# Performance work log

Hardware: AMD Instinct MI355X
Metric: run time of the kernel (lower is better)

The kernel has to match this reference:

```python
import jax, jax.numpy as jnp
import numpy as np

L, N, E, H, D, F = 2048, 2, 1024, 16, 64, 4096  # seq, batch, embed, heads, head_dim, ffn
EPS = 1e-5


def _ln(x, w, b):
    m = jnp.mean(x, axis=-1, keepdims=True)
    v = jnp.mean(jnp.square(x - m), axis=-1, keepdims=True)
    return (x - m) * jax.lax.rsqrt(v + EPS) * w + b


def setup_inputs() -> dict:
    key = jax.random.key(0)
    ks = jax.random.split(key, 16)
    s = 0.02
    f32 = jnp.float32
    return {
        "x": jax.random.normal(ks[0], (L, N, E), f32),
        "ln1_w": jnp.ones((E,), f32),
        "ln1_b": jnp.zeros((E,), f32),
        "wq": jax.random.normal(ks[1], (H * D, E), f32) * s,
        "bq": jnp.zeros((H * D,), f32),
        "wk": jax.random.normal(ks[2], (H * D, E), f32) * s,
        "bk": jnp.zeros((H * D,), f32),
        "wv": jax.random.normal(ks[3], (H * D, E), f32) * s,
        "bv": jnp.zeros((H * D,), f32),
        "wout": jax.random.normal(ks[4], (E, H * D), f32) * s,
        "bout": jnp.zeros((E,), f32),
        "ln2_w": jnp.ones((E,), f32),
        "ln2_b": jnp.zeros((E,), f32),
        "fc1_w": jax.random.normal(ks[5], (F, E), f32) * s,
        "fc1_b": jnp.zeros((F,), f32),
        "fc2_w": jax.random.normal(ks[6], (E, F), f32) * s,
        "fc2_b": jnp.zeros((E,), f32),
    }


def reference(x, ln1_w, ln1_b, wq, bq, wk, bk, wv, bv, wout, bout,
              ln2_w, ln2_b, fc1_w, fc1_b, fc2_w, fc2_b):
    scale = D ** (-0.5)
    residual = x
    h = _ln(x, ln1_w, ln1_b)                      # (L,N,E)
    q = (h @ wq.T + bq).reshape(L, N, H, D) * scale
    k = (h @ wk.T + bk).reshape(L, N, H, D)
    v = (h @ wv.T + bv).reshape(L, N, H, D)
    attn = jnp.einsum('qnhd,knhd->nhqk', q, k)    # (N,H,L,L) full score matrix
    causal = jnp.tril(jnp.ones((L, L), bool))
    attn = jnp.where(causal[None, None], attn, jnp.float32(-10000.0))
    p = jax.nn.softmax(attn, axis=-1)
    o = jnp.einsum('nhqk,knhd->qnhd', p, v).reshape(L, N, H * D)
    o = o @ wout.T + bout
    x = o + residual
    residual = x
    h = _ln(x, ln2_w, ln2_b)
    h = jax.nn.gelu(h @ fc1_w.T + fc1_b, approximate=False)
    h = h @ fc2_w.T + fc2_b
    return h + residual
```

## Files before the change

### kernel.cpp

```cpp
#include <hip/hip_runtime.h>
#include <hip/hip_bf16.h>
#include <math.h>

using bf16 = __hip_bfloat16;
typedef __bf16 bf16x8 __attribute__((ext_vector_type(8)));
typedef short  short4v __attribute__((ext_vector_type(4)));
typedef float  f32x4  __attribute__((ext_vector_type(4)));

static constexpr int Lq = 2048, Nb = 2, E = 1024, Hh = 16, Dd = 64, Ff = 4096;
static constexpr int MT = Lq * Nb;
static constexpr int QKLD = 2 * E;
static constexpr int LDL = 2 * QKLD;

__device__ __forceinline__ void async_lds16(const void* g, void* l) {
  __builtin_amdgcn_global_load_lds(
      (const __attribute__((address_space(1))) void*)g,
      (__attribute__((address_space(3))) void*)l, 16, 0, 0);
}
__device__ __forceinline__ bf16x8 ld8(const bf16* p) { return *(const bf16x8*)p; }
__device__ __forceinline__ short bfbits(float x) {
  bf16 t = __float2bfloat16(x);
  return *(short*)&t;
}

__global__ __launch_bounds__(256) void cvt_all_kernel(
    const float* __restrict__ wq, const float* __restrict__ wk,
    const float* __restrict__ wv, const float* __restrict__ wout,
    const float* __restrict__ fc1w, const float* __restrict__ fc2w,
    bf16* __restrict__ wqkvb, bf16* __restrict__ woutb,
    bf16* __restrict__ f1wb, bf16* __restrict__ f2wb) {
  const int i = blockIdx.x * 256 + threadIdx.x;
  const float* src;
  bf16* dst;
  size_t off;
  if (i < 786432) {
    const int r = i >> 18;
    off = (size_t)(i & 262143);
    src = (r == 0) ? wq : (r == 1) ? wk : wv;
    dst = wqkvb + (size_t)r * (E * E);
  } else if (i < 1048576) {
    off = (size_t)(i - 786432); src = wout; dst = woutb;
  } else if (i < 2097152) {
    off = (size_t)(i - 1048576); src = fc1w; dst = f1wb;
  } else {
    off = (size_t)(i - 2097152); src = fc2w; dst = f2wb;
  }
  float4 v = ((const float4*)src)[off];
  bf16 o4[4] = {__float2bfloat16(v.x), __float2bfloat16(v.y),
                __float2bfloat16(v.z), __float2bfloat16(v.w)};
  *(uint2*)(dst + 4 * off) = *(uint2*)o4;
}

template <int EPI>
__global__ __launch_bounds__(256) void gemm_bt(
    const bf16* __restrict__ A, const bf16* __restrict__ W,
    const float* __restrict__ b1, const float* __restrict__ b2,
    const float* __restrict__ b3, int Klen, int Kstride, int Nld,
    float qscale, int scut, bf16* __restrict__ outb,
    bf16* __restrict__ outv) {
  __shared__ __align__(16) bf16 As[128 * 32];
  __shared__ __align__(16) bf16 Bs[128 * 32];
  const int tid = threadIdx.x;
  const int w = tid >> 6, lane = tid & 63;
  const int quad = lane >> 4, l16 = lane & 15;
  const int wm = (w >> 1) * 64, wn = (w & 1) * 64;
  const int m0 = blockIdx.y * 128, n0 = blockIdx.x * 128;
  const int koff = blockIdx.z * Klen;

  f32x4 acc[4][4];
#pragma unroll
  for (int i = 0; i < 4; i++)
#pragma unroll
    for (int j = 0; j < 4; j++)
#pragma unroll
      for (int r = 0; r < 4; r++) acc[i][j][r] = 0.f;

  const int c0 = w * 64 + lane;
  const int c1 = c0 + 256;
  const size_t arow0 = (size_t)(m0 + (c0 >> 2)), arow1 = (size_t)(m0 + (c1 >> 2));
  const size_t brow0 = (size_t)(n0 + (c0 >> 2)), brow1 = (size_t)(n0 + (c1 >> 2));
  const int col0 = (c0 & 3) * 8, col1 = (c1 & 3) * 8;
  bf16* ldsA0 = &As[(w * 64) * 8];
  bf16* ldsA1 = &As[(256 + w * 64) * 8];
  bf16* ldsB0 = &Bs[(w * 64) * 8];
  bf16* ldsB1 = &Bs[(256 + w * 64) * 8];

  const int nk = Klen >> 5;
  for (int kt = 0; kt < nk; ++kt) {
    const int k0 = koff + kt * 32;
    async_lds16(A + arow0 * Kstride + k0 + col0, ldsA0);
    async_lds16(A + arow1 * Kstride + k0 + col1, ldsA1);
    async_lds16(W + brow0 * Kstride + k0 + col0, ldsB0);
    async_lds16(W + brow1 * Kstride + k0 + col1, ldsB1);
    __syncthreads();
    bf16x8 a[4], b[4];
#pragma unroll
    for (int i = 0; i < 4; i++) {
      a[i] = ld8(&As[(wm + i * 16 + l16) * 32 + quad * 8]);
      b[i] = ld8(&Bs[(wn + i * 16 + l16) * 32 + quad * 8]);
    }
#pragma unroll
    for (int i = 0; i < 4; i++)
#pragma unroll
      for (int j = 0; j < 4; j++)
        acc[i][j] = __builtin_amdgcn_mfma_f32_16x16x32_bf16(a[i], b[j], acc[i][j], 0, 0, 0);
    __syncthreads();
  }

  const size_t zoff = (EPI == 3) ? (size_t)blockIdx.z * ((size_t)MT * E) : 0;
#pragma unroll
  for (int i = 0; i < 4; i++) {
    const int mrow = m0 + wm + i * 16 + quad * 4;
#pragma unroll
    for (int j = 0; j < 4; j++) {
      const int ncol = n0 + wn + j * 16 + l16;
      float bv = 0.f;
      if constexpr (EPI != 3) {
        if (b3 != nullptr) {
          bv = (ncol < 1024) ? b1[ncol]
               : (ncol < 2048) ? b2[ncol - 1024] : b3[ncol - 2048];
        } else {
          bv = b1[ncol];
        }
      }
      const float sc = (ncol < scut) ? qscale : 1.0f;
#pragma unroll
      for (int r = 0; r < 4; r++) {
        float v = (acc[i][j][r] + bv) * sc;
        if constexpr (EPI == 2) {
          v = 0.5f * v * (1.f + erff(v * 0.70710678118f));
          outb[(size_t)(mrow + r) * Nld + ncol] = __float2bfloat16(v);
        } else if constexpr (EPI == 3) {
          outb[zoff + (size_t)(mrow + r) * Nld + ncol] = __float2bfloat16(v);
        } else {
          if (ncol < 2048) {
            outb[(size_t)(mrow + r) * 2048 + ncol] = __float2bfloat16(v);
          } else {
            const int h = (ncol - 2048) >> 6, d = ncol & 63;
            const int tok = mrow + r, n = tok & 1, l = tok >> 1;
            outv[(size_t)((n * 16 + h) * 64 + d) * Lq + l] = __float2bfloat16(v);
          }
        }
      }
    }
  }
}

__global__ __launch_bounds__(256) void reduce2_kernel(
    const bf16* __restrict__ P, const float* __restrict__ bias,
    const float* __restrict__ res, float* __restrict__ out) {
  const int i = blockIdx.x * 256 + threadIdx.x;
  const size_t e0 = (size_t)i * 4;
  const int col = (int)(e0 & (E - 1));
  uint2 u0 = *(const uint2*)(P + e0);
  uint2 u1 = *(const uint2*)(P + (size_t)MT * E + e0);
  const bf16* p0 = (const bf16*)&u0;
  const bf16* p1 = (const bf16*)&u1;
  float4 b = *(const float4*)(bias + col);
  float4 r = *(const float4*)(res + e0);
  float4 o;
  o.x = (float)p0[0] + (float)p1[0] + b.x + r.x;
  o.y = (float)p0[1] + (float)p1[1] + b.y + r.y;
  o.z = (float)p0[2] + (float)p1[2] + b.z + r.z;
  o.w = (float)p0[3] + (float)p1[3] + b.w + r.w;
  *(float4*)(out + e0) = o;
}

__global__ __launch_bounds__(256) void ln_kernel(
    const float* __restrict__ x, const float* __restrict__ wgt,
    const float* __restrict__ bia, bf16* __restrict__ out) {
  const int t = blockIdx.x, tid = threadIdx.x;
  const size_t base = (size_t)t * E;
  float v4[4], s = 0.f, ss = 0.f;
#pragma unroll
  for (int i = 0; i < 4; i++) {
    float v = x[base + i * 256 + tid];
    v4[i] = v; s += v; ss += v * v;
  }
  for (int off = 32; off > 0; off >>= 1) {
    s += __shfl_down(s, off, 64);
    ss += __shfl_down(ss, off, 64);
  }
  __shared__ float rs[4], rss[4], mv[2];
  const int w = tid >> 6;
  if ((tid & 63) == 0) { rs[w] = s; rss[w] = ss; }
  __syncthreads();
  if (tid == 0) {
    float S = rs[0] + rs[1] + rs[2] + rs[3];
    float SS = rss[0] + rss[1] + rss[2] + rss[3];
    float mean = S * (1.f / E);
    float var = SS * (1.f / E) - mean * mean;
    mv[0] = mean; mv[1] = rsqrtf(var + 1e-5f);
  }
  __syncthreads();
  const float mean = mv[0], rstd = mv[1];
#pragma unroll
  for (int i = 0; i < 4; i++) {
    const int e = i * 256 + tid;
    float r = (v4[i] - mean) * rstd * wgt[e] + bia[e];
    out[base + e] = __float2bfloat16(r);
  }
}

__global__ __launch_bounds__(256) void attn_kernel(
    const bf16* __restrict__ QK, const bf16* __restrict__ VT,
    bf16* __restrict__ O) {
  __shared__ __align__(16) bf16 KB[512 * 8];
  __shared__ __align__(16) bf16 VB[512 * 8];
  const int tid = threadIdx.x;
  const int w = tid >> 6, lane = tid & 63, quad = lane >> 4, l16 = lane & 15;
  const int pid = blockIdx.x;
  const int hh = blockIdx.y;
  const int n = hh >> 4, h = hh & 15;

  const bf16* Qp = QK + n * QKLD + h * Dd;
  const bf16* Kp = Qp + E;
  const bf16* Vp = VT + (size_t)hh * 64 * Lq;

  bf16* ldsK0 = KB + (size_t)(w * 64) * 8;
  bf16* ldsK1 = KB + (size_t)(256 + w * 64) * 8;
  bf16* ldsV0 = VB + (size_t)(w * 64) * 8;
  bf16* ldsV1 = VB + (size_t)(256 + w * 64) * 8;
  const int w8 = w * 8;

  for (int half = 0; half < 2; ++half) {
    const int qt = (half == 0) ? (31 - pid) : pid;
    const int ql = qt * 64 + w * 16 + l16;
    const bf16x8 aq0 = ld8(Qp + (size_t)ql * LDL + quad * 8);
    const bf16x8 aq1 = ld8(Qp + (size_t)ql * LDL + 32 + quad * 8);

    f32x4 o_acc[4];
#pragma unroll
    for (int d = 0; d < 4; d++)
#pragma unroll
      for (int r = 0; r < 4; r++) o_acc[d][r] = 0.f;
    float m_run = -3e30f, l_run = 0.f;

    for (int kt = 0; kt <= qt; ++kt) {
      const size_t kb = (size_t)kt * 64;

      async_lds16(Kp + (size_t)(kb + lane) * LDL + w8, ldsK0);
      async_lds16(Kp + (size_t)(kb + lane) * LDL + 32 + w8, ldsK1);
      async_lds16(Vp + (size_t)lane * Lq + kb + w8, ldsV0);
      async_lds16(Vp + (size_t)lane * Lq + kb + 32 + w8, ldsV1);
      __syncthreads();

      f32x4 s[4];
#pragma unroll
      for (int ks = 0; ks < 4; ks++) {
        const bf16x8 kc0 = ld8(&KB[(size_t)((quad)*64 + ks * 16 + l16) * 8]);
        const bf16x8 kc1 = ld8(&KB[(size_t)((4 + quad) * 64 + ks * 16 + l16) * 8]);
#pragma unroll
        for (int r = 0; r < 4; r++) s[ks][r] = 0.f;
        s[ks] = __builtin_amdgcn_mfma_f32_16x16x32_bf16(kc0, aq0, s[ks], 0, 0, 0);
        s[ks] = __builtin_amdgcn_mfma_f32_16x16x32_bf16(kc1, aq1, s[ks], 0, 0, 0);
      }

      if (kt == qt) {
#pragma unroll
        for (int ks = 0; ks < 4; ks++) {
#pragma unroll
          for (int r = 0; r < 4; r++) {
            const int kg = kt * 64 + ks * 16 + quad * 4 + r;
            if (kg > ql) s[ks][r] = -14427.0f;
          }
        }
      }

      float tmax = s[0][0];
#pragma unroll
      for (int ks = 0; ks < 4; ks++)
#pragma unroll
        for (int r = 0; r < 4; r++) tmax = fmaxf(tmax, s[ks][r]);
      tmax = fmaxf(tmax, __shfl_xor(tmax, 16, 64));
      tmax = fmaxf(tmax, __shfl_xor(tmax, 32, 64));
      const float mnew = fmaxf(m_run, tmax);
      const float alpha = exp2f(m_run - mnew);
      m_run = mnew;
      float rsum = 0.f;
      short4v pf[4];
#pragma unroll
      for (int ks = 0; ks < 4; ks++) {
#pragma unroll
        for (int r = 0; r < 4; r++) {
          const float pv = exp2f(s[ks][r] - mnew);
          rsum += pv;
          pf[ks][r] = bfbits(pv);
        }
      }
      rsum += __shfl_xor(rsum, 16, 64);
      rsum += __shfl_xor(rsum, 32, 64);
      l_run = l_run * alpha + rsum;
#pragma unroll
      for (int d = 0; d < 4; d++)
#pragma unroll
        for (int r = 0; r < 4; r++) o_acc[d][r] *= alpha;

#pragma unroll
      for (int d = 0; d < 4; d++) {
#pragma unroll
        for (int ks = 0; ks < 4; ks++) {
          const int g = ks * 2 + (quad >> 1);
          const short4v av =
              *(const short4v*)&VB[(size_t)(g * 64 + d * 16 + l16) * 8 + (quad & 1) * 4];
          o_acc[d] = __builtin_amdgcn_mfma_f32_16x16x16bf16_1k(av, pf[ks], o_acc[d], 0, 0, 0);
        }
      }
      __syncthreads();
    }

    const float inv_l = 1.f / fmaxf(l_run, 1e-30f);
    const size_t obase = (size_t)ql * (Nb * E) + (size_t)n * E + h * Dd;
#pragma unroll
    for (int d = 0; d < 4; d++)
#pragma unroll
      for (int r = 0; r < 4; r++)
        O[obase + d * 16 + quad * 4 + r] = __float2bfloat16(o_acc[d][r] * inv_l);
  }
}

extern "C" void kernel_launch(void* const* d_in, const int* in_sizes, int n_in,
                              void* d_out, int out_size, void* d_ws, size_t ws_size,
                              hipStream_t stream) {
  const float* x    = (const float*)d_in[0];
  const float* ln1w = (const float*)d_in[1];
  const float* ln1b = (const float*)d_in[2];
  const float* wq   = (const float*)d_in[3];
  const float* bq   = (const float*)d_in[4];
  const float* wk   = (const float*)d_in[5];
  const float* bk   = (const float*)d_in[6];
  const float* wv   = (const float*)d_in[7];
  const float* bv   = (const float*)d_in[8];
  const float* wout = (const float*)d_in[9];
  const float* bout = (const float*)d_in[10];
  const float* ln2w = (const float*)d_in[11];
  const float* ln2b = (const float*)d_in[12];
  const float* fc1w = (const float*)d_in[13];
  const float* fc1b = (const float*)d_in[14];
  const float* fc2w = (const float*)d_in[15];
  const float* fc2b = (const float*)d_in[16];

  char* ws = (char*)d_ws;
  bf16* wqkvb = (bf16*)(ws);
  bf16* woutb = (bf16*)(ws + ((size_t)6 << 20));
  bf16* f1wb  = (bf16*)(ws + ((size_t)8 << 20));
  bf16* f2wb  = (bf16*)(ws + ((size_t)16 << 20));
  bf16* h1    = (bf16*)(ws + ((size_t)24 << 20));
  bf16* qk    = (bf16*)(ws + ((size_t)32 << 20));
  bf16* vtg   = (bf16*)(ws + ((size_t)48 << 20));
  bf16* o     = (bf16*)(ws + ((size_t)56 << 20));
  float* x1   = (float*)(ws + ((size_t)64 << 20));
  bf16* Pout  = (bf16*)(ws + ((size_t)32 << 20));
  bf16* P01   = (bf16*)(ws);
  bf16* f1    = (bf16*)(ws + ((size_t)32 << 20));
  bf16* h2    = h1;
  float* outp = (float*)d_out;

  cvt_all_kernel<<<12288, 256, 0, stream>>>(wq, wk, wv, wout, fc1w, fc2w,
                                            wqkvb, woutb, f1wb, f2wb);

  ln_kernel<<<MT, 256, 0, stream>>>(x, ln1w, ln1b, h1);

  dim3 gQKV(3 * E / 128, MT / 128);
  dim3 gE2(E / 128, MT / 128, 2);
  dim3 gF(Ff / 128, MT / 128);

  gemm_bt<4><<<gQKV, 256, 0, stream>>>(h1, wqkvb, bq, bk, bv, E, E, 2048,
                                       0.125f * 1.44269504f, 1024, qk, vtg);

  attn_kernel<<<dim3(16, Nb * Hh), 256, 0, stream>>>(qk, vtg, o);

  gemm_bt<3><<<gE2, 256, 0, stream>>>(o, woutb, nullptr, nullptr, nullptr,
                                      E / 2, E, E, 1.f, 0, Pout, nullptr);
  reduce2_kernel<<<MT * E / 1024, 256, 0, stream>>>(Pout, bout, x, x1);

  ln_kernel<<<MT, 256, 0, stream>>>(x1, ln2w, ln2b, h2);

  gemm_bt<2><<<gF, 256, 0, stream>>>(h2, f1wb, fc1b, nullptr, nullptr, E, E, Ff,
                                     1.f, 0, f1, nullptr);

  gemm_bt<3><<<gE2, 256, 0, stream>>>(f1, f2wb, nullptr, nullptr, nullptr,
                                      Ff / 2, Ff, E, 1.f, 0, P01, nullptr);
  reduce2_kernel<<<MT * E / 1024, 256, 0, stream>>>(P01, fc2b, x1, outp);
}
```

Before: 423.2 us.

## Deepen GEMM K-tile with swizzled LDS, fuse reduce+LN2, use tanh-form GELU

```diff
diff --git a/kernel.cpp b/kernel.cpp
--- a/kernel.cpp
+++ b/kernel.cpp
@@ -21,6 +21,11 @@
 __device__ __forceinline__ short bfbits(float x) {
   bf16 t = __float2bfloat16(x);
   return *(short*)&t;
+}
+__device__ __forceinline__ float gelu_fast(float v) {
+  const float y = fminf(2.302208f * (v + 0.044715f * v * v * v), 80.f);
+  const float t = exp2f(y);
+  return v * t / (t + 1.0f);
 }
 
 __global__ __launch_bounds__(256) void cvt_all_kernel(
@@ -58,8 +63,8 @@
     const float* __restrict__ b3, int Klen, int Kstride, int Nld,
     float qscale, int scut, bf16* __restrict__ outb,
     bf16* __restrict__ outv) {
-  __shared__ __align__(16) bf16 As[128 * 32];
-  __shared__ __align__(16) bf16 Bs[128 * 32];
+  __shared__ __align__(16) bf16 As[128 * 64];
+  __shared__ __align__(16) bf16 Bs[128 * 64];
   const int tid = threadIdx.x;
   const int w = tid >> 6, lane = tid & 63;
   const int quad = lane >> 4, l16 = lane & 15;
@@ -75,35 +80,37 @@
 #pragma unroll
       for (int r = 0; r < 4; r++) acc[i][j][r] = 0.f;
 
-  const int c0 = w * 64 + lane;
-  const int c1 = c0 + 256;
-  const size_t arow0 = (size_t)(m0 + (c0 >> 2)), arow1 = (size_t)(m0 + (c1 >> 2));
-  const size_t brow0 = (size_t)(n0 + (c0 >> 2)), brow1 = (size_t)(n0 + (c1 >> 2));
-  const int col0 = (c0 & 3) * 8, col1 = (c1 & 3) * 8;
-  bf16* ldsA0 = &As[(w * 64) * 8];
-  bf16* ldsA1 = &As[(256 + w * 64) * 8];
-  bf16* ldsB0 = &Bs[(w * 64) * 8];
-  bf16* ldsB1 = &Bs[(256 + w * 64) * 8];
-
-  const int nk = Klen >> 5;
+  const int rowoff = w * 8 + (lane >> 3);
+  const int colsw = (((lane & 7) ^ (lane >> 3)) << 3);
+
+  const int nk = Klen >> 6;
   for (int kt = 0; kt < nk; ++kt) {
-    const int k0 = koff + kt * 32;
-    async_lds16(A + arow0 * Kstride + k0 + col0, ldsA0);
-    async_lds16(A + arow1 * Kstride + k0 + col1, ldsA1);
-    async_lds16(W + brow0 * Kstride + k0 + col0, ldsB0);
-    async_lds16(W + brow1 * Kstride + k0 + col1, ldsB1);
+    const int k0 = koff + (kt << 6);
+#pragma unroll
+    for (int r = 0; r < 4; r++) {
+      async_lds16(A + (size_t)(m0 + r * 32 + rowoff) * Kstride + k0 + colsw,
+                  As + (size_t)(r * 256 + w * 64) * 8);
+      async_lds16(W + (size_t)(n0 + r * 32 + rowoff) * Kstride + k0 + colsw,
+                  Bs + (size_t)(r * 256 + w * 64) * 8);
+    }
     __syncthreads();
-    bf16x8 a[4], b[4];
-#pragma unroll
-    for (int i = 0; i < 4; i++) {
-      a[i] = ld8(&As[(wm + i * 16 + l16) * 32 + quad * 8]);
-      b[i] = ld8(&Bs[(wn + i * 16 + l16) * 32 + quad * 8]);
+#pragma unroll
+    for (int ksub = 0; ksub < 2; ksub++) {
+      const int gx = ksub * 4 + quad;
+      bf16x8 a[4], b[4];
+#pragma unroll
+      for (int i = 0; i < 4; i++) {
+        const int ra = wm + i * 16 + l16;
+        const int rb = wn + i * 16 + l16;
+        a[i] = ld8(&As[(size_t)(ra * 8 + (gx ^ (l16 & 7))) * 8]);
+        b[i] = ld8(&Bs[(size_t)(rb * 8 + (gx ^ (l16 & 7))) * 8]);
+      }
+#pragma unroll
+      for (int i = 0; i < 4; i++)
+#pragma unroll
+        for (int j = 0; j < 4; j++)
+          acc[i][j] = __builtin_amdgcn_mfma_f32_16x16x32_bf16(a[i], b[j], acc[i][j], 0, 0, 0);
     }
-#pragma unroll
-    for (int i = 0; i < 4; i++)
-#pragma unroll
-      for (int j = 0; j < 4; j++)
-        acc[i][j] = __builtin_amdgcn_mfma_f32_16x16x32_bf16(a[i], b[j], acc[i][j], 0, 0, 0);
     __syncthreads();
   }
 
@@ -128,8 +135,7 @@
       for (int r = 0; r < 4; r++) {
         float v = (acc[i][j][r] + bv) * sc;
         if constexpr (EPI == 2) {
-          v = 0.5f * v * (1.f + erff(v * 0.70710678118f));
-          outb[(size_t)(mrow + r) * Nld + ncol] = __float2bfloat16(v);
+          outb[(size_t)(mrow + r) * Nld + ncol] = __float2bfloat16(gelu_fast(v));
         } else if constexpr (EPI == 3) {
           outb[zoff + (size_t)(mrow + r) * Nld + ncol] = __float2bfloat16(v);
         } else {
@@ -164,6 +170,57 @@
   o.z = (float)p0[2] + (float)p1[2] + b.z + r.z;
   o.w = (float)p0[3] + (float)p1[3] + b.w + r.w;
   *(float4*)(out + e0) = o;
+}
+
+__global__ __launch_bounds__(256) void redln_kernel(
+    const bf16* __restrict__ P, const float* __restrict__ bias,
+    const float* __restrict__ res, const float* __restrict__ wgt,
+    const float* __restrict__ bia, float* __restrict__ x1,
+    bf16* __restrict__ h2) {
+  const int t = blockIdx.x, tid = threadIdx.x;
+  const size_t base = (size_t)t * E;
+  const int e0 = tid * 4;
+  uint2 u0 = *(const uint2*)(P + base + e0);
+  uint2 u1 = *(const uint2*)(P + (size_t)MT * E + base + e0);
+  const bf16* p0 = (const bf16*)&u0;
+  const bf16* p1 = (const bf16*)&u1;
+  float4 b = *(const float4*)(bias + e0);
+  float4 r = *(const float4*)(res + base + e0);
+  float v4[4];
+  v4[0] = (float)p0[0] + (float)p1[0] + b.x + r.x;
+  v4[1] = (float)p0[1] + (float)p1[1] + b.y + r.y;
+  v4[2] = (float)p0[2] + (float)p1[2] + b.z + r.z;
+  v4[3] = (float)p0[3] + (float)p1[3] + b.w + r.w;
+  *(float4*)(x1 + base + e0) = *(float4*)v4;
+
+  float s = 0.f, ss = 0.f;
+#pragma unroll
+  for (int i = 0; i < 4; i++) { s += v4[i]; ss += v4[i] * v4[i]; }
+  for (int off = 32; off > 0; off >>= 1) {
+    s += __shfl_down(s, off, 64);
+    ss += __shfl_down(ss, off, 64);
+  }
+  __shared__ float rs[4], rss[4], mv[2];
+  const int w = tid >> 6;
+  if ((tid & 63) == 0) { rs[w] = s; rss[w] = ss; }
+  __syncthreads();
+  if (tid == 0) {
+    float S = rs[0] + rs[1] + rs[2] + rs[3];
+    float SS = rss[0] + rss[1] + rss[2] + rss[3];
+    float mean = S * (1.f / E);
+    float var = SS * (1.f / E) - mean * mean;
+    mv[0] = mean; mv[1] = rsqrtf(var + 1e-5f);
+  }
+  __syncthreads();
+  const float mean = mv[0], rstd = mv[1];
+  float4 wg = *(const float4*)(wgt + e0);
+  float4 bb = *(const float4*)(bia + e0);
+  bf16 o4[4];
+  o4[0] = __float2bfloat16((v4[0] - mean) * rstd * wg.x + bb.x);
+  o4[1] = __float2bfloat16((v4[1] - mean) * rstd * wg.y + bb.y);
+  o4[2] = __float2bfloat16((v4[2] - mean) * rstd * wg.z + bb.z);
+  o4[3] = __float2bfloat16((v4[3] - mean) * rstd * wg.w + bb.w);
+  *(uint2*)(h2 + base + e0) = *(uint2*)o4;
 }
 
 __global__ __launch_bounds__(256) void ln_kernel(
@@ -372,9 +429,7 @@
 
   gemm_bt<3><<<gE2, 256, 0, stream>>>(o, woutb, nullptr, nullptr, nullptr,
                                       E / 2, E, E, 1.f, 0, Pout, nullptr);
-  reduce2_kernel<<<MT * E / 1024, 256, 0, stream>>>(Pout, bout, x, x1);
-
-  ln_kernel<<<MT, 256, 0, stream>>>(x1, ln2w, ln2b, h2);
+  redln_kernel<<<MT, 256, 0, stream>>>(Pout, bout, x, ln2w, ln2b, x1, h2);
 
   gemm_bt<2><<<gF, 256, 0, stream>>>(h2, f1wb, fc1b, nullptr, nullptr, E, E, Ff,
                                      1.f, 0, f1, nullptr);
```

Measured after the change: 380.5 us. -10.1%, faster.
